# Kernel tuning notes

Hardware: AMD Instinct MI355X
Metric: run time of the kernel (lower is better)

The kernel has to match this reference:

```python
import jax, jax.numpy as jnp
import numpy as np

B, LQ, LK, D, H, DK, DV = 8, 1024, 1024, 512, 8, 64, 64
EPS = 1e-14          # K.epsilon()**2 with default K.epsilon()=1e-7
MASK_VALUE = -1e30   # default mask_value in call()


def setup_inputs() -> dict:
    key = jax.random.key(0)
    ks = jax.random.split(key, 7)
    query = jax.random.normal(ks[0], (B, LQ, D), jnp.float32)
    key_t = jax.random.normal(ks[1], (B, LK, D), jnp.float32)
    value = jax.random.normal(ks[2], (B, LK, D), jnp.float32)
    mask = jax.random.randint(ks[3], (B, LK), 0, 2).astype(jnp.float32)
    glorot = np.sqrt(2.0 / (D + DK)).astype(np.float32)
    Wq = jax.random.normal(ks[4], (H, D, DK), jnp.float32) * glorot
    Wk = jax.random.normal(ks[5], (H, D, DK), jnp.float32) * glorot
    Wv = jax.random.normal(ks[6], (H, D, DV), jnp.float32) * glorot
    gamma = jnp.ones((1,), jnp.float32)
    beta = jnp.zeros((1,), jnp.float32)
    return {"query": query, "key": key_t, "value": value, "mask": mask,
            "Wq": Wq, "Wk": Wk, "Wv": Wv, "gamma": gamma, "beta": beta}


def reference(query, key, value, mask, Wq, Wk, Wv, gamma, beta):
    # Per-head projections (the original's Python loop over heads, vectorized).
    q = jnp.einsum('bqd,hde->bhqe', query, Wq)   # [B,H,LQ,DK]
    k = jnp.einsum('bkd,hde->bhke', key, Wk)     # [B,H,LK,DK]
    v = jnp.einsum('bkd,hde->bhke', value, Wv)   # [B,H,LK,DV]
    # NOTE: no 1/sqrt(dk) scaling, faithful to the source.
    A = jnp.einsum('bhqe,bhke->bhqk', q, k)      # [B,H,LQ,LK]
    m = mask[:, None, None, :]                    # [B,1,1,LK] broadcast over heads & queries
    A = m * A + (1.0 - m) * MASK_VALUE
    A = jax.nn.softmax(A, axis=-1)
    o = jnp.einsum('bhqk,bhke->bhqe', A, v)      # [B,H,LQ,DV]
    conc = o.transpose(0, 2, 1, 3).reshape(B, LQ, H * DV)  # concat heads
    # Scalar-affine layernorm over the concatenated feature dim.
    mean = jnp.mean(conc, axis=-1, keepdims=True)
    var = jnp.mean(jnp.square(conc - mean), axis=-1, keepdims=True)
    x = (conc - mean) / jnp.sqrt(var + EPS)
    return x * gamma[0] + beta[0]
```

## Files before the change

kernel.cpp:

```cpp
#include <hip/hip_runtime.h>
#include <math.h>

#define NB 8
#define NLQ 1024
#define NLK 1024
#define ND 512
#define NH 8
#define MASKV -1e30f
#define LOG2E 1.44269504088896f
#define SHIFT2 32.0f

typedef unsigned short ushort_t;
typedef __attribute__((ext_vector_type(8))) _Float16 f16x8;
typedef __attribute__((ext_vector_type(8))) short bf16x8;
typedef __attribute__((ext_vector_type(16))) float f32x16;

__device__ __forceinline__ ushort_t f2h_bits(float f) {
    union { _Float16 h; ushort_t u; } v; v.h = (_Float16)f;
    return v.u;
}
__device__ __forceinline__ ushort_t f2bf(float f) {
    union { float f; unsigned u; } v; v.f = f;
    unsigned r = v.u + 0x7fffu + ((v.u >> 16) & 1u);
    return (ushort_t)(r >> 16);
}
__device__ __forceinline__ void gload16(const ushort_t* g, ushort_t* l) {
    __builtin_amdgcn_global_load_lds(
        (const __attribute__((address_space(1))) void*)g,
        (__attribute__((address_space(3))) void*)l, 16, 0, 0);
}
__device__ __forceinline__ unsigned pack_bf16_trunc(float p0, float p1) {
    return __builtin_amdgcn_perm(__float_as_uint(p1), __float_as_uint(p0),
                                 0x07060302u);
}

__global__ __launch_bounds__(256) void wsplit_kernel(
    const float* __restrict__ Wq, const float* __restrict__ Wk, const float* __restrict__ Wv,
    ushort_t* __restrict__ oq, ushort_t* __restrict__ ok, ushort_t* __restrict__ ov) {
    __shared__ float T[64][65];
    const int d0 = blockIdx.x * 64;
    const int h  = blockIdx.y;
    const int t  = blockIdx.z;
    const float* W = (t == 0) ? Wq : (t == 1) ? Wk : Wv;
    ushort_t* oh = (t == 0) ? oq : (t == 1) ? ok : ov;
    const float scale = (t == 0) ? LOG2E : 1.f;
    const int tid = threadIdx.x;
#pragma unroll
    for (int i = 0; i < 4; i++) {
        int r = (tid >> 4) + i * 16;
        int c = (tid & 15) * 4;
        float4 v = *(const float4*)&W[((size_t)h * ND + d0 + r) * 64 + c];
        *(float4*)&T[r][c] = v;
    }
    __syncthreads();
    const int e = tid & 63;
    const int dg = tid >> 6;
    ushort_t hs[16];
#pragma unroll
    for (int dd = 0; dd < 16; dd++) hs[dd] = f2h_bits(T[dg * 16 + dd][e] * scale);
    size_t base = ((size_t)h * 64 + e) * ND + d0 + dg * 16;
#pragma unroll
    for (int c = 0; c < 2; c++) {
        uint4 wh;
        wh.x = (unsigned)hs[8*c+0] | ((unsigned)hs[8*c+1] << 16);
        wh.y = (unsigned)hs[8*c+2] | ((unsigned)hs[8*c+3] << 16);
        wh.z = (unsigned)hs[8*c+4] | ((unsigned)hs[8*c+5] << 16);
        wh.w = (unsigned)hs[8*c+6] | ((unsigned)hs[8*c+7] << 16);
        *(uint4*)&oh[base + 8 * c] = wh;
    }
}

__global__ __launch_bounds__(256) void xcvt_kernel(
    const float* __restrict__ Xq, const float* __restrict__ Xk, const float* __restrict__ Xv,
    ushort_t* __restrict__ obase) {
    const int t = blockIdx.z;
    const float* X = (t == 0) ? Xq : (t == 1) ? Xk : Xv;
    ushort_t* o = obase + (size_t)t * ((size_t)NB * NLQ * ND);
    const size_t i = ((size_t)blockIdx.x * 256 + threadIdx.x) * 8;
    float4 a = *(const float4*)&X[i];
    float4 b = *(const float4*)&X[i + 4];
    ushort_t hs[8];
    hs[0] = f2h_bits(a.x); hs[1] = f2h_bits(a.y);
    hs[2] = f2h_bits(a.z); hs[3] = f2h_bits(a.w);
    hs[4] = f2h_bits(b.x); hs[5] = f2h_bits(b.y);
    hs[6] = f2h_bits(b.z); hs[7] = f2h_bits(b.w);
    uint4 wh;
    wh.x = (unsigned)hs[0] | ((unsigned)hs[1] << 16);
    wh.y = (unsigned)hs[2] | ((unsigned)hs[3] << 16);
    wh.z = (unsigned)hs[4] | ((unsigned)hs[5] << 16);
    wh.w = (unsigned)hs[6] | ((unsigned)hs[7] << 16);
    *(uint4*)&o[i] = wh;
}

__global__ __launch_bounds__(256, 4) void proj_mfma_kernel(
    const ushort_t* __restrict__ Xc, const ushort_t* __restrict__ Wbase,
    ushort_t* __restrict__ Obase) {
    __shared__ ushort_t sX[2][4160];
    __shared__ ushort_t sW[2][4160];

    const int l0 = blockIdx.x * 64;
    const int h  = blockIdx.y;
    const int z  = blockIdx.z;
    const int t  = z >> 3;
    const int b  = z & 7;
    const int tid  = threadIdx.x;
    const int wave = tid >> 6;
    const int lane = tid & 63;
    const int l31  = lane & 31;
    const int hib  = lane >> 5;
    const size_t bh = (size_t)b * NH + h;

    const ushort_t* gx = Xc + (size_t)t * ((size_t)NB * NLQ * ND)
                       + ((size_t)b * NLQ + l0) * ND;
    const ushort_t* gw = Wbase + (size_t)t * ((size_t)NH * 64 * ND)
                       + (size_t)h * 64 * ND;
    ushort_t* out = Obase + (size_t)t * ((size_t)NB * NH * NLQ * 64);

    const int srow = lane >> 3;
    const int schk = (lane & 7) ^ srow;

    auto stage = [&](int buf, int d0) {
#pragma unroll
        for (int i = 0; i < 2; i++) {
            int u = i * 4 + wave;
            int row = u * 8 + srow;
            gload16(gx + (size_t)row * ND + d0 + schk * 8, sX[buf] + u * 520);
            gload16(gw + (size_t)row * ND + d0 + schk * 8, sW[buf] + u * 520);
        }
    };

    f32x16 acc;
#pragma unroll
    for (int i = 0; i < 16; i++) acc[i] = 0.f;

    const int arow = (wave >> 1) * 32 + l31;
    const int brow = (wave & 1) * 32 + l31;
    const int apad = (arow >> 3) * 520 + (arow & 7) * 64;
    const int bpad = (brow >> 3) * 520 + (brow & 7) * 64;
    const int sw = l31 & 7;

    stage(0, 0);
    __syncthreads();
    int cur = 0;
    for (int kc = 0; kc < 8; kc++) {
        if (kc < 7) stage(cur ^ 1, (kc + 1) * 64);
#pragma unroll
        for (int c = 0; c < 4; c++) {
            const int pc = ((2 * c + hib) ^ sw) * 8;
            f16x8 xh = *(const f16x8*)&sX[cur][apad + pc];
            f16x8 wh = *(const f16x8*)&sW[cur][bpad + pc];
            acc = __builtin_amdgcn_mfma_f32_32x32x16_f16(xh, wh, acc, 0, 0, 0);
        }
        __syncthreads();
        cur ^= 1;
    }

    if (t < 2) {
        const size_t obase = (bh * NLQ + l0) * 64;
        const int e = (wave & 1) * 32 + l31;
#pragma unroll
        for (int r = 0; r < 16; r++) {
            int l = (wave >> 1) * 32 + (r & 3) + 8 * (r >> 2) + 4 * hib;
            out[obase + (size_t)l * 64 + e] = f2h_bits(acc[r]);
        }
    } else {
        ushort_t (*T)[68] = (ushort_t(*)[68])sX;
        const int e = (wave & 1) * 32 + l31;
#pragma unroll
        for (int r = 0; r < 16; r++) {
            int l = (wave >> 1) * 32 + (r & 3) + 8 * (r >> 2) + 4 * hib;
            T[e][l] = f2bf(acc[r]);
        }
        __syncthreads();
        const int e2 = tid >> 2;
        const int lc = (tid & 3) * 16;
        size_t base = (bh * 64 + e2) * NLK + l0 + lc;
        *(uint4*)&out[base]     = *(const uint4*)&T[e2][lc];
        *(uint4*)&out[base + 8] = *(const uint4*)&T[e2][lc + 8];
    }
}

__global__ __launch_bounds__(256, 4) void attn_kernel(
    const ushort_t* __restrict__ Qf, const ushort_t* __restrict__ Kf,
    const ushort_t* __restrict__ Vt, const float* __restrict__ maskp,
    float* __restrict__ Op) {
    __shared__ ushort_t sK[2][4160];
    __shared__ ushort_t sV[2][4160];
    __shared__ float sBias[1024];

    const int idx = blockIdx.x;
    const int bh_i = idx & 63;
    const int qc  = idx >> 6;
    const int b = bh_i >> 3, h = bh_i & 7;
    const size_t bh = (size_t)b * NH + h;

    const int tid  = threadIdx.x;
    const int wave = tid >> 6;
    const int lane = tid & 63;
    const int l31  = lane & 31;
    const int hib  = lane >> 5;
    const int q = qc * 128 + wave * 32 + l31;
    const int sw = l31 & 7;

    {
        const float* mrow = maskp + ((size_t)b << 10);
        float4 m0 = *(const float4*)&mrow[tid * 4];
        float4 bi;
        bi.x = (m0.x > 0.5f) ? -SHIFT2 : MASKV;
        bi.y = (m0.y > 0.5f) ? -SHIFT2 : MASKV;
        bi.z = (m0.z > 0.5f) ? -SHIFT2 : MASKV;
        bi.w = (m0.w > 0.5f) ? -SHIFT2 : MASKV;
        *(float4*)&sBias[tid * 4] = bi;
    }

    f16x8 qh[4];
    {
        const ushort_t* ph = Qf + (bh * NLQ + q) * 64 + hib * 8;
#pragma unroll
        for (int c = 0; c < 4; c++) qh[c] = *(const f16x8*)(ph + c * 16);
    }

    const int srow = lane >> 3;
    const int schk = (lane & 7) ^ srow;

    auto stage = [&](int buf, int k0) {
#pragma unroll
        for (int n = 0; n < 4; n++) {
            int u = wave + n * 4;
            if (u < 8) {
                int row = u * 8 + srow;
                int key = (row & ~12) | ((row & 4) << 1) | ((row & 8) >> 1);
                gload16(Kf + ((bh << 10) + k0 + key) * 64 + schk * 8,
                        sK[buf] + u * 520);
            } else {
                int u8 = u - 8;
                int row = u8 * 8 + srow;
                gload16(Vt + ((bh << 6) + row) * NLK + k0 + schk * 8,
                        sV[buf] + u8 * 520);
            }
        }
    };

    f32x16 O0, O1;
#pragma unroll
    for (int i = 0; i < 16; i++) { O0[i] = 0.f; O1[i] = 0.f; }
    float lrun = 0.f;

    const int rp0 = (l31 >> 3) * 520 + (l31 & 7) * 64;
    const int rp1 = rp0 + 4 * 520;

    stage(0, 0);
    __syncthreads();
    int cur = 0;

    for (int t = 0; t < 16; t++) {
        const int k0 = t << 6;
        if (t < 15) stage(cur ^ 1, k0 + 64);

        f32x16 S0, S1;
#pragma unroll
        for (int g = 0; g < 4; g++) {
            const int kb = k0 + 16 * (g >> 1) + 8 * hib + 4 * (g & 1);
            float4 b0 = *(const float4*)&sBias[kb];
            float4 b1 = *(const float4*)&sBias[kb + 32];
            S0[4 * g + 0] = b0.x; S0[4 * g + 1] = b0.y;
            S0[4 * g + 2] = b0.z; S0[4 * g + 3] = b0.w;
            S1[4 * g + 0] = b1.x; S1[4 * g + 1] = b1.y;
            S1[4 * g + 2] = b1.z; S1[4 * g + 3] = b1.w;
        }
#pragma unroll
        for (int c = 0; c < 4; c++) {
            const int pc = ((2 * c + hib) ^ sw) * 8;
            f16x8 a0 = *(const f16x8*)&sK[cur][rp0 + pc];
            f16x8 a1 = *(const f16x8*)&sK[cur][rp1 + pc];
            S0 = __builtin_amdgcn_mfma_f32_32x32x16_f16(a0, qh[c], S0, 0, 0, 0);
            S1 = __builtin_amdgcn_mfma_f32_32x32x16_f16(a1, qh[c], S1, 0, 0, 0);
        }

        unsigned pq[8][2];
#pragma unroll
        for (int g = 0; g < 8; g++) {
            float p0, p1, p2, p3;
            if (g < 4) {
                p0 = __builtin_amdgcn_exp2f(S0[4*g+0]);
                p1 = __builtin_amdgcn_exp2f(S0[4*g+1]);
                p2 = __builtin_amdgcn_exp2f(S0[4*g+2]);
                p3 = __builtin_amdgcn_exp2f(S0[4*g+3]);
            } else {
                p0 = __builtin_amdgcn_exp2f(S1[4*(g-4)+0]);
                p1 = __builtin_amdgcn_exp2f(S1[4*(g-4)+1]);
                p2 = __builtin_amdgcn_exp2f(S1[4*(g-4)+2]);
                p3 = __builtin_amdgcn_exp2f(S1[4*(g-4)+3]);
            }
            lrun += (p0 + p1) + (p2 + p3);
            pq[g][0] = pack_bf16_trunc(p0, p1);
            pq[g][1] = pack_bf16_trunc(p2, p3);
        }

#pragma unroll
        for (int c = 0; c < 4; c++) {
            union { unsigned u[4]; bf16x8 v; } pf;
            pf.u[0] = pq[2 * c][0];     pf.u[1] = pq[2 * c][1];
            pf.u[2] = pq[2 * c + 1][0]; pf.u[3] = pq[2 * c + 1][1];
            const int pc = ((2 * c + hib) ^ sw) * 8;
            bf16x8 v0 = *(const bf16x8*)&sV[cur][rp0 + pc];
            bf16x8 v1 = *(const bf16x8*)&sV[cur][rp1 + pc];
            O0 = __builtin_amdgcn_mfma_f32_32x32x16_bf16(v0, pf.v, O0, 0, 0, 0);
            O1 = __builtin_amdgcn_mfma_f32_32x32x16_bf16(v1, pf.v, O1, 0, 0, 0);
        }
        __syncthreads();
        cur ^= 1;
    }

    lrun += __shfl_xor(lrun, 32);
    const float linv = 1.f / lrun;
    float* obase = Op + ((size_t)(b * NLQ + q)) * (NH * 64) + h * 64;
#pragma unroll
    for (int me = 0; me < 2; me++) {
#pragma unroll
        for (int g = 0; g < 4; g++) {
            int e0 = me * 32 + 8 * g + 4 * hib;
            float4 o;
            if (me == 0) {
                o.x = O0[4 * g + 0] * linv; o.y = O0[4 * g + 1] * linv;
                o.z = O0[4 * g + 2] * linv; o.w = O0[4 * g + 3] * linv;
            } else {
                o.x = O1[4 * g + 0] * linv; o.y = O1[4 * g + 1] * linv;
                o.z = O1[4 * g + 2] * linv; o.w = O1[4 * g + 3] * linv;
            }
            *(float4*)&obase[e0] = o;
        }
    }
}

__global__ __launch_bounds__(256) void ln_kernel(const float* __restrict__ X,
                                                 const float* __restrict__ gamma,
                                                 const float* __restrict__ beta,
                                                 float* __restrict__ out) {
    const int row = blockIdx.x * 4 + (threadIdx.x >> 6);
    const int lane = threadIdx.x & 63;
    const float* x = &X[(size_t)row * 512];
    float4 v0 = *(const float4*)&x[lane * 8];
    float4 v1 = *(const float4*)&x[lane * 8 + 4];
    float sum = v0.x + v0.y + v0.z + v0.w + v1.x + v1.y + v1.z + v1.w;
    float sq = v0.x * v0.x + v0.y * v0.y + v0.z * v0.z + v0.w * v0.w
             + v1.x * v1.x + v1.y * v1.y + v1.z * v1.z + v1.w * v1.w;
#pragma unroll
    for (int off = 32; off > 0; off >>= 1) {
        sum += __shfl_down(sum, off);
        sq  += __shfl_down(sq, off);
    }
    sum = __shfl(sum, 0);
    sq  = __shfl(sq, 0);
    const float mean = sum * (1.f / 512.f);
    const float var = sq * (1.f / 512.f) - mean * mean;
    const float rstd = rsqrtf(var + 1e-14f);
    const float g = gamma[0], be = beta[0];
    float* o = &out[(size_t)row * 512];
    float4 r0, r1;
    r0.x = (v0.x - mean) * rstd * g + be;  r0.y = (v0.y - mean) * rstd * g + be;
    r0.z = (v0.z - mean) * rstd * g + be;  r0.w = (v0.w - mean) * rstd * g + be;
    r1.x = (v1.x - mean) * rstd * g + be;  r1.y = (v1.y - mean) * rstd * g + be;
    r1.z = (v1.z - mean) * rstd * g + be;  r1.w = (v1.w - mean) * rstd * g + be;
    *(float4*)&o[lane * 8] = r0;
    *(float4*)&o[lane * 8 + 4] = r1;
}

extern "C" void kernel_launch(void* const* d_in, const int* in_sizes, int n_in,
                              void* d_out, int out_size, void* d_ws, size_t ws_size,
                              hipStream_t stream) {
    const float* query = (const float*)d_in[0];
    const float* key_t = (const float*)d_in[1];
    const float* value = (const float*)d_in[2];
    const float* mask  = (const float*)d_in[3];
    const float* Wq    = (const float*)d_in[4];
    const float* Wk    = (const float*)d_in[5];
    const float* Wv    = (const float*)d_in[6];
    const float* gamma = (const float*)d_in[7];
    const float* beta  = (const float*)d_in[8];
    float* out = (float*)d_out;

    const size_t A = (size_t)NB * NLQ * ND;
    const size_t WS = (size_t)NH * 64 * ND;
    ushort_t* Qf = (ushort_t*)d_ws;
    ushort_t* Kf = Qf + A;
    ushort_t* Vt = Qf + 2 * A;
    ushort_t* Xc = Qf + 3 * A;
    ushort_t* Wt = Qf + 6 * A;

    wsplit_kernel<<<dim3(ND / 64, NH, 3), 256, 0, stream>>>(
        Wq, Wk, Wv, Wt, Wt + WS, Wt + 2 * WS);

    xcvt_kernel<<<dim3((unsigned)(A / 2048), 1, 3), 256, 0, stream>>>(
        query, key_t, value, Xc);

    proj_mfma_kernel<<<dim3(NLQ / 64, NH, 24), 256, 0, stream>>>(Xc, Wt, Qf);

    attn_kernel<<<512, 256, 0, stream>>>(Qf, Kf, Vt, mask, out);

    ln_kernel<<<(NB * NLQ) / 4, 256, 0, stream>>>(out, gamma, beta, out);
}
```

Before: 170.7 us.

## Merge conversion kernels and split attention into 64-query, two-wave blocks

Folds the weight transpose/convert and input convert kernels into one prep kernel, removing a launch. Attention blocks now hold 2 waves covering 64 queries instead of 4 waves covering 128, giving 1024 blocks instead of 512 for better spread across CUs. Each wave now stages both K and V tiles. The trade-off is that each K/V tile is loaded twice as often in total, since fewer queries share each staged tile.

```diff
diff --git a/kernel.cpp b/kernel.cpp
--- a/kernel.cpp
+++ b/kernel.cpp
@@ -34,17 +34,33 @@
                                  0x07060302u);
 }
 
-__global__ __launch_bounds__(256) void wsplit_kernel(
+__global__ __launch_bounds__(256) void prep_kernel(
+    const float* __restrict__ Xq, const float* __restrict__ Xk, const float* __restrict__ Xv,
     const float* __restrict__ Wq, const float* __restrict__ Wk, const float* __restrict__ Wv,
-    ushort_t* __restrict__ oq, ushort_t* __restrict__ ok, ushort_t* __restrict__ ov) {
+    ushort_t* __restrict__ xobase, ushort_t* __restrict__ wobase) {
     __shared__ float T[64][65];
-    const int d0 = blockIdx.x * 64;
-    const int h  = blockIdx.y;
-    const int t  = blockIdx.z;
+    const int t = blockIdx.z;
+    const int tid = threadIdx.x;
+    if (blockIdx.x < 2048) {
+        const float* X = (t == 0) ? Xq : (t == 1) ? Xk : Xv;
+        ushort_t* o = xobase + (size_t)t * ((size_t)NB * NLQ * ND);
+        const size_t i = ((size_t)blockIdx.x * 256 + tid) * 8;
+        float4 a = *(const float4*)&X[i];
+        float4 b = *(const float4*)&X[i + 4];
+        uint4 wh;
+        wh.x = (unsigned)f2h_bits(a.x) | ((unsigned)f2h_bits(a.y) << 16);
+        wh.y = (unsigned)f2h_bits(a.z) | ((unsigned)f2h_bits(a.w) << 16);
+        wh.z = (unsigned)f2h_bits(b.x) | ((unsigned)f2h_bits(b.y) << 16);
+        wh.w = (unsigned)f2h_bits(b.z) | ((unsigned)f2h_bits(b.w) << 16);
+        *(uint4*)&o[i] = wh;
+        return;
+    }
+    const int i2 = blockIdx.x - 2048;
+    const int d0 = (i2 & 7) * 64;
+    const int h  = i2 >> 3;
     const float* W = (t == 0) ? Wq : (t == 1) ? Wk : Wv;
-    ushort_t* oh = (t == 0) ? oq : (t == 1) ? ok : ov;
+    ushort_t* oh = wobase + (size_t)t * ((size_t)NH * 64 * ND);
     const float scale = (t == 0) ? LOG2E : 1.f;
-    const int tid = threadIdx.x;
 #pragma unroll
     for (int i = 0; i < 4; i++) {
         int r = (tid >> 4) + i * 16;
@@ -68,28 +84,6 @@
         wh.w = (unsigned)hs[8*c+6] | ((unsigned)hs[8*c+7] << 16);
         *(uint4*)&oh[base + 8 * c] = wh;
     }
-}
-
-__global__ __launch_bounds__(256) void xcvt_kernel(
-    const float* __restrict__ Xq, const float* __restrict__ Xk, const float* __restrict__ Xv,
-    ushort_t* __restrict__ obase) {
-    const int t = blockIdx.z;
-    const float* X = (t == 0) ? Xq : (t == 1) ? Xk : Xv;
-    ushort_t* o = obase + (size_t)t * ((size_t)NB * NLQ * ND);
-    const size_t i = ((size_t)blockIdx.x * 256 + threadIdx.x) * 8;
-    float4 a = *(const float4*)&X[i];
-    float4 b = *(const float4*)&X[i + 4];
-    ushort_t hs[8];
-    hs[0] = f2h_bits(a.x); hs[1] = f2h_bits(a.y);
-    hs[2] = f2h_bits(a.z); hs[3] = f2h_bits(a.w);
-    hs[4] = f2h_bits(b.x); hs[5] = f2h_bits(b.y);
-    hs[6] = f2h_bits(b.z); hs[7] = f2h_bits(b.w);
-    uint4 wh;
-    wh.x = (unsigned)hs[0] | ((unsigned)hs[1] << 16);
-    wh.y = (unsigned)hs[2] | ((unsigned)hs[3] << 16);
-    wh.z = (unsigned)hs[4] | ((unsigned)hs[5] << 16);
-    wh.w = (unsigned)hs[6] | ((unsigned)hs[7] << 16);
-    *(uint4*)&o[i] = wh;
 }
 
 __global__ __launch_bounds__(256, 4) void proj_mfma_kernel(
@@ -180,7 +174,7 @@
     }
 }
 
-__global__ __launch_bounds__(256, 4) void attn_kernel(
+__global__ __launch_bounds__(128, 2) void attn_kernel(
     const ushort_t* __restrict__ Qf, const ushort_t* __restrict__ Kf,
     const ushort_t* __restrict__ Vt, const float* __restrict__ maskp,
     float* __restrict__ Op) {
@@ -199,18 +193,24 @@
     const int lane = tid & 63;
     const int l31  = lane & 31;
     const int hib  = lane >> 5;
-    const int q = qc * 128 + wave * 32 + l31;
+    const int q = qc * 64 + wave * 32 + l31;
     const int sw = l31 & 7;
 
     {
         const float* mrow = maskp + ((size_t)b << 10);
-        float4 m0 = *(const float4*)&mrow[tid * 4];
-        float4 bi;
-        bi.x = (m0.x > 0.5f) ? -SHIFT2 : MASKV;
-        bi.y = (m0.y > 0.5f) ? -SHIFT2 : MASKV;
-        bi.z = (m0.z > 0.5f) ? -SHIFT2 : MASKV;
-        bi.w = (m0.w > 0.5f) ? -SHIFT2 : MASKV;
-        *(float4*)&sBias[tid * 4] = bi;
+        float4 m0 = *(const float4*)&mrow[tid * 8];
+        float4 m1 = *(const float4*)&mrow[tid * 8 + 4];
+        float4 b0, b1;
+        b0.x = (m0.x > 0.5f) ? -SHIFT2 : MASKV;
+        b0.y = (m0.y > 0.5f) ? -SHIFT2 : MASKV;
+        b0.z = (m0.z > 0.5f) ? -SHIFT2 : MASKV;
+        b0.w = (m0.w > 0.5f) ? -SHIFT2 : MASKV;
+        b1.x = (m1.x > 0.5f) ? -SHIFT2 : MASKV;
+        b1.y = (m1.y > 0.5f) ? -SHIFT2 : MASKV;
+        b1.z = (m1.z > 0.5f) ? -SHIFT2 : MASKV;
+        b1.w = (m1.w > 0.5f) ? -SHIFT2 : MASKV;
+        *(float4*)&sBias[tid * 8]     = b0;
+        *(float4*)&sBias[tid * 8 + 4] = b1;
     }
 
     f16x8 qh[4];
@@ -226,18 +226,13 @@
     auto stage = [&](int buf, int k0) {
 #pragma unroll
         for (int n = 0; n < 4; n++) {
-            int u = wave + n * 4;
-            if (u < 8) {
-                int row = u * 8 + srow;
-                int key = (row & ~12) | ((row & 4) << 1) | ((row & 8) >> 1);
-                gload16(Kf + ((bh << 10) + k0 + key) * 64 + schk * 8,
-                        sK[buf] + u * 520);
-            } else {
-                int u8 = u - 8;
-                int row = u8 * 8 + srow;
-                gload16(Vt + ((bh << 6) + row) * NLK + k0 + schk * 8,
-                        sV[buf] + u8 * 520);
-            }
+            int u = wave * 4 + n;
+            int row = u * 8 + srow;
+            int key = (row & ~12) | ((row & 4) << 1) | ((row & 8) >> 1);
+            gload16(Kf + ((bh << 10) + k0 + key) * 64 + schk * 8,
+                    sK[buf] + u * 520);
+            gload16(Vt + ((bh << 6) + row) * NLK + k0 + schk * 8,
+                    sV[buf] + u * 520);
         }
     };
 
@@ -388,15 +383,12 @@
     ushort_t* Xc = Qf + 3 * A;
     ushort_t* Wt = Qf + 6 * A;
 
-    wsplit_kernel<<<dim3(ND / 64, NH, 3), 256, 0, stream>>>(
-        Wq, Wk, Wv, Wt, Wt + WS, Wt + 2 * WS);
-
-    xcvt_kernel<<<dim3((unsigned)(A / 2048), 1, 3), 256, 0, stream>>>(
-        query, key_t, value, Xc);
+    prep_kernel<<<dim3(2048 + 64, 1, 3), 256, 0, stream>>>(
+        query, key_t, value, Wq, Wk, Wv, Xc, Wt);
 
     proj_mfma_kernel<<<dim3(NLQ / 64, NH, 24), 256, 0, stream>>>(Xc, Wt, Qf);
 
-    attn_kernel<<<512, 256, 0, stream>>>(Qf, Kf, Vt, mask, out);
+    attn_kernel<<<1024, 128, 0, stream>>>(Qf, Kf, Vt, mask, out);
 
     ln_kernel<<<(NB * NLQ) / 4, 256, 0, stream>>>(out, gamma, beta, out);
 }
```

New measurement: 170.2 us. About the same (-0.3%).
